# Kernel tuning notes

Hardware: AMD Instinct MI355X
Metric: run time of the kernel (lower is better)

## Reference

```python
import jax, jax.numpy as jnp
import numpy as np

B, T, D, H = 32, 1024, 512, 512


def setup_inputs() -> dict:
    key = jax.random.key(0)
    k = jax.random.split(key, 5)
    s = 1.0 / np.sqrt(H)  # PyTorch LSTM init scale U(-1/sqrt(H), 1/sqrt(H))
    return {
        "x": jax.random.normal(k[0], (B, T, D), dtype=jnp.float32),
        "W_ih": jax.random.uniform(k[1], (4 * H, D), jnp.float32, -s, s),
        "W_hh": jax.random.uniform(k[2], (4 * H, H), jnp.float32, -s, s),
        "b_ih": jax.random.uniform(k[3], (4 * H,), jnp.float32, -s, s),
        "b_hh": jax.random.uniform(k[4], (4 * H,), jnp.float32, -s, s),
    }


def _lstm(x, W_ih, W_hh, b_ih, b_hh):
    # x: [B, T, D] (batch_first). Precompute input projections for all steps.
    xg = jnp.einsum("btd,gd->btg", x, W_ih) + (b_ih + b_hh)  # [B, T, 4H]
    xg = jnp.transpose(xg, (1, 0, 2))  # [T, B, 4H] time-major for scan

    def step(carry, xg_t):
        h, c = carry  # [B, H] each
        gates = xg_t + h @ W_hh.T  # [B, 4H]
        i, f, g, o = jnp.split(gates, 4, axis=-1)  # PyTorch gate order i,f,g,o
        i = jax.nn.sigmoid(i)
        f = jax.nn.sigmoid(f)
        g = jnp.tanh(g)
        o = jax.nn.sigmoid(o)
        c = f * c + i * g
        h = o * jnp.tanh(c)
        return (h, c), h

    h0 = jnp.zeros((x.shape[0], H), x.dtype)
    c0 = jnp.zeros((x.shape[0], H), x.dtype)
    (h_n, c_n), hs = jax.lax.scan(step, (h0, c0), xg)
    out = jnp.transpose(hs, (1, 0, 2))  # [B, T, H] batch_first output
    return out, h_n[None], c_n[None]  # h_n/c_n: [num_layers=1, B, H]


def reference(x, W_ih, W_hh, b_ih, b_hh):
    # Returns (last_hidden_state, h_n, c_n) matching outputs[0], outputs[1]
    return _lstm(x, W_ih, W_hh, b_ih, b_hh)
```

## Files before the change

kernel.cpp:

```cpp
#include <hip/hip_runtime.h>
#include <stdint.h>

typedef __attribute__((ext_vector_type(4))) float f32x4;
typedef __attribute__((ext_vector_type(8))) short bf16x8;
typedef __attribute__((ext_vector_type(4))) unsigned int u32x4;
typedef __attribute__((ext_vector_type(2))) unsigned int u32x2;
typedef __attribute__((ext_vector_type(4))) unsigned short u16x4;
typedef unsigned short ushort_t;

#define B_N 32
#define T_N 1024
#define D_N 512
#define H_N 512
#define G4H 2048

__device__ __forceinline__ ushort_t f2bf(float f) {
    union { float f; unsigned int u; } v; v.f = f;
    unsigned int r = v.u + 0x7FFFu + ((v.u >> 16) & 1u);
    return (ushort_t)(r >> 16);
}
__device__ __forceinline__ float bf2f(ushort_t b) {
    union { unsigned int u; float f; } v; v.u = ((unsigned int)b) << 16;
    return v.f;
}
__device__ __forceinline__ float fsig(float x) {
    return __builtin_amdgcn_rcpf(1.f + __expf(-x));
}
__device__ __forceinline__ float ftanh(float x) {
    return 1.f - 2.f * __builtin_amdgcn_rcpf(1.f + __expf(2.f * x));
}

__global__ __launch_bounds__(256) void prep_kernel(
    const float* __restrict__ wih, const float* __restrict__ whh,
    const float* __restrict__ bih, const float* __restrict__ bhh,
    ushort_t* __restrict__ wihb, ushort_t* __restrict__ whhb,
    float* __restrict__ bias, unsigned int* __restrict__ ringu)
{
    size_t i = (size_t)blockIdx.x * 256 + threadIdx.x;
    if (i < 2048) bias[i] = bih[i] + bhh[i];
    if (i < 32768) ringu[i] = 0u;
    const size_t NW = (size_t)G4H * D_N / 4;
    if (i < NW) {
        f32x4 v = ((const f32x4*)wih)[i];
        u16x4 o; o[0]=f2bf(v[0]); o[1]=f2bf(v[1]); o[2]=f2bf(v[2]); o[3]=f2bf(v[3]);
        ((u16x4*)wihb)[i] = o;
    } else if (i < 2 * NW) {
        size_t j = i - NW;
        f32x4 v = ((const f32x4*)whh)[j];
        u16x4 o; o[0]=f2bf(v[0]); o[1]=f2bf(v[1]); o[2]=f2bf(v[2]); o[3]=f2bf(v[3]);
        ((u16x4*)whhb)[j] = o;
    }
}

__global__ __launch_bounds__(512, 1) void xg_gemm(
    const float* __restrict__ x,
    const ushort_t* __restrict__ wihb,
    const float* __restrict__ bias,
    ushort_t* __restrict__ xg)
{
    const int tc = blockIdx.x >> 3;
    const int gb = blockIdx.x & 7;
    const int tid = threadIdx.x;
    const int w = tid >> 6, l = tid & 63, lr = l & 15, lk = l >> 4;

    __shared__ ushort_t xs[16 * 520];

    const int r0 = gb * 256 + w * 16;
    const int r1 = r0 + 128;
    bf16x8 a0[16], a1[16];
#pragma unroll
    for (int kk = 0; kk < 16; ++kk) {
        a0[kk] = *(const bf16x8*)(wihb + (size_t)(r0 + lr) * D_N + kk * 32 + lk * 8);
        a1[kk] = *(const bf16x8*)(wihb + (size_t)(r1 + lr) * D_N + kk * 32 + lk * 8);
    }
    float bs0[4], bs1[4];
#pragma unroll
    for (int j = 0; j < 4; ++j) {
        bs0[j] = bias[r0 + lk * 4 + j];
        bs1[j] = bias[r1 + lk * 4 + j];
    }

    const int srow = tid >> 5;
    const int sq   = tid & 31;

    for (int b = 0; b < B_N; ++b) {
        const float* xr = x + ((size_t)b * T_N + tc * 16 + srow) * D_N;
#pragma unroll
        for (int c = 0; c < 4; ++c) {
            f32x4 v = *(const f32x4*)(xr + c * 128 + sq * 4);
            u16x4 o; o[0]=f2bf(v[0]); o[1]=f2bf(v[1]); o[2]=f2bf(v[2]); o[3]=f2bf(v[3]);
            *(u16x4*)(xs + srow * 520 + c * 128 + sq * 4) = o;
        }
        __syncthreads();

        f32x4 c0, c1;
#pragma unroll
        for (int j = 0; j < 4; ++j) { c0[j] = 0.f; c1[j] = 0.f; }
#pragma unroll
        for (int kk = 0; kk < 16; ++kk) {
            bf16x8 bf = *(const bf16x8*)((const char*)xs + lr * 1040 + kk * 64 + lk * 16);
            c0 = __builtin_amdgcn_mfma_f32_16x16x32_bf16(a0[kk], bf, c0, 0, 0, 0);
            c1 = __builtin_amdgcn_mfma_f32_16x16x32_bf16(a1[kk], bf, c1, 0, 0, 0);
        }

        const int t = tc * 16 + lr;
        ushort_t* op = xg + (size_t)t * (B_N * G4H) + (size_t)b * G4H;
        u16x4 o0, o1;
#pragma unroll
        for (int j = 0; j < 4; ++j) {
            o0[j] = f2bf(c0[j] + bs0[j]);
            o1[j] = f2bf(c1[j] + bs1[j]);
        }
        *(u16x4*)(op + r0 + lk * 4) = o0;
        *(u16x4*)(op + r1 + lk * 4) = o1;
        __syncthreads();
    }
}

__global__ __launch_bounds__(512, 1) void lstm_rec(
    const ushort_t* __restrict__ xg,
    const ushort_t* __restrict__ whhb,
    unsigned int* __restrict__ ringu,
    float* __restrict__ out,
    float* __restrict__ hn,
    float* __restrict__ cn)
{
    const int tid = threadIdx.x;
    const int g = blockIdx.x >> 4;
    const int s = blockIdx.x & 15;
    const int w = tid >> 6, l = tid & 63, lr = l & 15, lk = l >> 4;

    __shared__ ushort_t hstage[4][544];

    const int col4 = s * 32 + w * 4;
    const int gc = (lr >> 2) * 512 + col4 + (lr & 3);
    bf16x8 wfrag[16];
#pragma unroll
    for (int kk = 0; kk < 16; ++kk)
        wfrag[kk] = *(const bf16x8*)(whhb + (size_t)gc * H_N + kk * 32 + lk * 8);

    float c_reg[4] = {0.f, 0.f, 0.f, 0.f};
    unsigned int* ringg = ringu + g * 4096;
    const ushort_t* xgp = xg + (size_t)(g * 4) * G4H + gc;

    for (int t = 0; t < T_N; ++t) {
        const ushort_t* xa = xgp + (size_t)t * (B_N * G4H);
        f32x4 acc0, acc1;
#pragma unroll
        for (int j = 0; j < 4; ++j) {
            acc0[j] = bf2f(xa[(size_t)j * G4H]);
            acc1[j] = 0.f;
        }

        if (t > 0) {
            if (tid < 64) {
                const unsigned int* pp0 = ringg + ((t - 1) & 1) * 2048 + l * 8;
                const unsigned int* pp1 = pp0 + 1024;
                const unsigned int tp = ((unsigned int)t) << 16;
                u32x4 a[8];
                int guard = 0;
                for (;;) {
                    asm volatile(
                        "global_load_dwordx4 %0, %8, off sc0 sc1\n\t"
                        "global_load_dwordx4 %1, %8, off offset:16 sc0 sc1\n\t"
                        "global_load_dwordx4 %2, %8, off offset:2048 sc0 sc1\n\t"
                        "global_load_dwordx4 %3, %8, off offset:2064 sc0 sc1\n\t"
                        "global_load_dwordx4 %4, %9, off sc0 sc1\n\t"
                        "global_load_dwordx4 %5, %9, off offset:16 sc0 sc1\n\t"
                        "global_load_dwordx4 %6, %9, off offset:2048 sc0 sc1\n\t"
                        "global_load_dwordx4 %7, %9, off offset:2064 sc0 sc1\n\t"
                        "s_waitcnt vmcnt(0)"
                        : "=&v"(a[0]), "=&v"(a[1]), "=&v"(a[2]), "=&v"(a[3]),
                          "=&v"(a[4]), "=&v"(a[5]), "=&v"(a[6]), "=&v"(a[7])
                        : "v"(pp0), "v"(pp1)
                        : "memory");
                    unsigned int d = 0;
#pragma unroll
                    for (int r = 0; r < 8; ++r) {
                        d |= (a[r][0] ^ tp); d |= (a[r][1] ^ tp);
                        d |= (a[r][2] ^ tp); d |= (a[r][3] ^ tp);
                    }
                    int ok = ((d & 0xFFFF0000u) == 0u);
                    if (__all(ok) || ++guard > (1 << 16)) break;
                    __builtin_amdgcn_s_sleep(1);
                }
#pragma unroll
                for (int n = 0; n < 4; ++n) {
                    u32x4 p;
                    p[0] = __builtin_amdgcn_perm(a[2*n][1], a[2*n][0], 0x05040100u);
                    p[1] = __builtin_amdgcn_perm(a[2*n][3], a[2*n][2], 0x05040100u);
                    p[2] = __builtin_amdgcn_perm(a[2*n+1][1], a[2*n+1][0], 0x05040100u);
                    p[3] = __builtin_amdgcn_perm(a[2*n+1][3], a[2*n+1][2], 0x05040100u);
                    *(u32x4*)((char*)hstage + n * 1088 + l * 16) = p;
                }
            }
            __syncthreads();

            const char* ap = (const char*)hstage + (lr & 3) * 1088 + lk * 16;
#pragma unroll
            for (int kk = 0; kk < 16; ++kk) {
                bf16x8 af = *(const bf16x8*)(ap + kk * 64);
                if (kk & 1)
                    acc1 = __builtin_amdgcn_mfma_f32_16x16x32_bf16(af, wfrag[kk], acc1, 0, 0, 0);
                else
                    acc0 = __builtin_amdgcn_mfma_f32_16x16x32_bf16(af, wfrag[kk], acc0, 0, 0, 0);
            }
        } else {
            __syncthreads();
        }

#pragma unroll
        for (int j = 0; j < 4; ++j) acc0[j] += acc1[j];

        const int q = (l >> 2) & 3;
        float av[4];
#pragma unroll
        for (int j = 0; j < 4; ++j)
            av[j] = (q == 2) ? ftanh(acc0[j]) : fsig(acc0[j]);

        float hv[4];
#pragma unroll
        for (int j = 0; j < 4; ++j) {
            float f_ = __shfl_xor(av[j], 4);
            float g_ = __shfl_xor(av[j], 8);
            float o_ = __shfl_xor(av[j], 12);
            c_reg[j] = f_ * c_reg[j] + av[j] * g_;
            hv[j] = o_ * ftanh(c_reg[j]);
        }

        if (l < 4) {
            unsigned int* rp = ringg + (t & 1) * 2048 + col4 + l;
            const unsigned int tag = ((unsigned int)(t + 1)) << 16;
#pragma unroll
            for (int j = 0; j < 4; ++j) {
                unsigned int hw = tag | (unsigned int)f2bf(hv[j]);
                asm volatile("global_store_dword %0, %1, off sc0 sc1"
                             :: "v"(rp + j * 512), "v"(hw) : "memory");
            }
            float* op = out + (size_t)(g * 4) * T_N * H_N + (size_t)t * H_N + col4 + l;
#pragma unroll
            for (int j = 0; j < 4; ++j)
                op[(size_t)j * T_N * H_N] = hv[j];
            if (t == T_N - 1) {
#pragma unroll
                for (int j = 0; j < 4; ++j) {
                    size_t bi = (size_t)(g * 4 + j) * H_N + col4 + l;
                    hn[bi] = hv[j];
                    cn[bi] = c_reg[j];
                }
            }
        }
    }
}

extern "C" void kernel_launch(void* const* d_in, const int* in_sizes, int n_in,
                              void* d_out, int out_size, void* d_ws, size_t ws_size,
                              hipStream_t stream) {
    (void)in_sizes; (void)n_in; (void)out_size; (void)ws_size;
    const float* x   = (const float*)d_in[0];
    const float* wih = (const float*)d_in[1];
    const float* whh = (const float*)d_in[2];
    const float* bih = (const float*)d_in[3];
    const float* bhh = (const float*)d_in[4];
    float* out = (float*)d_out;
    float* hn  = out + (size_t)B_N * T_N * H_N;
    float* cn  = hn + (size_t)B_N * H_N;

    char* ws = (char*)d_ws;
    ushort_t*     xg    = (ushort_t*)    (ws);
    ushort_t*     wihb  = (ushort_t*)    (ws + 167772160);
    ushort_t*     whhb  = (ushort_t*)    (ws + 169869312);
    float*        bias  = (float*)       (ws + 171966464);
    unsigned int* ringu = (unsigned int*)(ws + 171974656);

    prep_kernel<<<2048, 256, 0, stream>>>(wih, whh, bih, bhh,
                                          wihb, whhb, bias, ringu);
    xg_gemm<<<512, 512, 0, stream>>>(x, wihb, bias, xg);
    lstm_rec<<<128, 512, 0, stream>>>(xg, whhb, ringu, out, hn, cn);
}
```

Before: 2.276 ms.

## Prefetch ring loads and next-step input gates before spin-wait

Issues the ring-buffer loads for the next timestep's hidden state right after storing the current h, and checks them at the top of the next step before falling back to the spin loop. Also prefetches the next step's precomputed input-gate values into registers. The MFMA accumulation is split across four independent accumulators instead of two to shorten dependency chains. The intent is to hide global-load and polling latency on the recurrent critical path. The prefetched ring loads may often return stale tags and trigger the retry path anyway, and the extra registers raise pressure.

```diff
diff --git a/kernel.cpp b/kernel.cpp
--- a/kernel.cpp
+++ b/kernel.cpp
@@ -143,46 +143,62 @@
     unsigned int* ringg = ringu + g * 4096;
     const ushort_t* xgp = xg + (size_t)(g * 4) * G4H + gc;
 
+    u32x4 a[8];
+    ushort_t xw[4];
+#pragma unroll
+    for (int j = 0; j < 4; ++j) xw[j] = xgp[(size_t)j * G4H];
+
     for (int t = 0; t < T_N; ++t) {
-        const ushort_t* xa = xgp + (size_t)t * (B_N * G4H);
-        f32x4 acc0, acc1;
+        f32x4 acc0, acc1, acc2, acc3;
 #pragma unroll
         for (int j = 0; j < 4; ++j) {
-            acc0[j] = bf2f(xa[(size_t)j * G4H]);
-            acc1[j] = 0.f;
+            acc0[j] = bf2f(xw[j]);
+            acc1[j] = 0.f; acc2[j] = 0.f; acc3[j] = 0.f;
         }
 
         if (t > 0) {
             if (tid < 64) {
-                const unsigned int* pp0 = ringg + ((t - 1) & 1) * 2048 + l * 8;
-                const unsigned int* pp1 = pp0 + 1024;
+                asm volatile("s_waitcnt vmcnt(0)"
+                             : "+v"(a[0]), "+v"(a[1]), "+v"(a[2]), "+v"(a[3]),
+                               "+v"(a[4]), "+v"(a[5]), "+v"(a[6]), "+v"(a[7])
+                             :: "memory");
                 const unsigned int tp = ((unsigned int)t) << 16;
-                u32x4 a[8];
-                int guard = 0;
-                for (;;) {
-                    asm volatile(
-                        "global_load_dwordx4 %0, %8, off sc0 sc1\n\t"
-                        "global_load_dwordx4 %1, %8, off offset:16 sc0 sc1\n\t"
-                        "global_load_dwordx4 %2, %8, off offset:2048 sc0 sc1\n\t"
-                        "global_load_dwordx4 %3, %8, off offset:2064 sc0 sc1\n\t"
-                        "global_load_dwordx4 %4, %9, off sc0 sc1\n\t"
-                        "global_load_dwordx4 %5, %9, off offset:16 sc0 sc1\n\t"
-                        "global_load_dwordx4 %6, %9, off offset:2048 sc0 sc1\n\t"
-                        "global_load_dwordx4 %7, %9, off offset:2064 sc0 sc1\n\t"
-                        "s_waitcnt vmcnt(0)"
-                        : "=&v"(a[0]), "=&v"(a[1]), "=&v"(a[2]), "=&v"(a[3]),
-                          "=&v"(a[4]), "=&v"(a[5]), "=&v"(a[6]), "=&v"(a[7])
-                        : "v"(pp0), "v"(pp1)
-                        : "memory");
-                    unsigned int d = 0;
-#pragma unroll
-                    for (int r = 0; r < 8; ++r) {
-                        d |= (a[r][0] ^ tp); d |= (a[r][1] ^ tp);
-                        d |= (a[r][2] ^ tp); d |= (a[r][3] ^ tp);
+                unsigned int d = 0;
+#pragma unroll
+                for (int r = 0; r < 8; ++r) {
+                    d |= (a[r][0] ^ tp); d |= (a[r][1] ^ tp);
+                    d |= (a[r][2] ^ tp); d |= (a[r][3] ^ tp);
+                }
+                int ok = ((d & 0xFFFF0000u) == 0u);
+                if (!__all(ok)) {
+                    const unsigned int* pp0 = ringg + ((t - 1) & 1) * 2048 + l * 8;
+                    const unsigned int* pp1 = pp0 + 1024;
+                    int guard = 0;
+                    for (;;) {
+                        __builtin_amdgcn_s_sleep(1);
+                        asm volatile(
+                            "global_load_dwordx4 %0, %8, off sc0 sc1\n\t"
+                            "global_load_dwordx4 %1, %8, off offset:16 sc0 sc1\n\t"
+                            "global_load_dwordx4 %2, %8, off offset:2048 sc0 sc1\n\t"
+                            "global_load_dwordx4 %3, %8, off offset:2064 sc0 sc1\n\t"
+                            "global_load_dwordx4 %4, %9, off sc0 sc1\n\t"
+                            "global_load_dwordx4 %5, %9, off offset:16 sc0 sc1\n\t"
+                            "global_load_dwordx4 %6, %9, off offset:2048 sc0 sc1\n\t"
+                            "global_load_dwordx4 %7, %9, off offset:2064 sc0 sc1\n\t"
+                            "s_waitcnt vmcnt(0)"
+                            : "=&v"(a[0]), "=&v"(a[1]), "=&v"(a[2]), "=&v"(a[3]),
+                              "=&v"(a[4]), "=&v"(a[5]), "=&v"(a[6]), "=&v"(a[7])
+                            : "v"(pp0), "v"(pp1)
+                            : "memory");
+                        d = 0;
+#pragma unroll
+                        for (int r = 0; r < 8; ++r) {
+                            d |= (a[r][0] ^ tp); d |= (a[r][1] ^ tp);
+                            d |= (a[r][2] ^ tp); d |= (a[r][3] ^ tp);
+                        }
+                        ok = ((d & 0xFFFF0000u) == 0u);
+                        if (__all(ok) || ++guard > (1 << 16)) break;
                     }
-                    int ok = ((d & 0xFFFF0000u) == 0u);
-                    if (__all(ok) || ++guard > (1 << 16)) break;
-                    __builtin_amdgcn_s_sleep(1);
                 }
 #pragma unroll
                 for (int n = 0; n < 4; ++n) {
@@ -200,17 +216,20 @@
 #pragma unroll
             for (int kk = 0; kk < 16; ++kk) {
                 bf16x8 af = *(const bf16x8*)(ap + kk * 64);
-                if (kk & 1)
-                    acc1 = __builtin_amdgcn_mfma_f32_16x16x32_bf16(af, wfrag[kk], acc1, 0, 0, 0);
-                else
-                    acc0 = __builtin_amdgcn_mfma_f32_16x16x32_bf16(af, wfrag[kk], acc0, 0, 0, 0);
+                switch (kk & 3) {
+                case 0: acc0 = __builtin_amdgcn_mfma_f32_16x16x32_bf16(af, wfrag[kk], acc0, 0, 0, 0); break;
+                case 1: acc1 = __builtin_amdgcn_mfma_f32_16x16x32_bf16(af, wfrag[kk], acc1, 0, 0, 0); break;
+                case 2: acc2 = __builtin_amdgcn_mfma_f32_16x16x32_bf16(af, wfrag[kk], acc2, 0, 0, 0); break;
+                default: acc3 = __builtin_amdgcn_mfma_f32_16x16x32_bf16(af, wfrag[kk], acc3, 0, 0, 0); break;
+                }
             }
         } else {
             __syncthreads();
         }
 
 #pragma unroll
-        for (int j = 0; j < 4; ++j) acc0[j] += acc1[j];
+        for (int j = 0; j < 4; ++j)
+            acc0[j] += (acc1[j] + acc2[j]) + acc3[j];
 
         const int q = (l >> 2) & 3;
         float av[4];
@@ -249,6 +268,29 @@
                     cn[bi] = c_reg[j];
                 }
             }
+        }
+
+        if (t < T_N - 1) {
+            if (tid < 64) {
+                const unsigned int* q0 = ringg + (t & 1) * 2048 + l * 8;
+                const unsigned int* q1 = q0 + 1024;
+                asm volatile(
+                    "global_load_dwordx4 %0, %8, off sc0 sc1\n\t"
+                    "global_load_dwordx4 %1, %8, off offset:16 sc0 sc1\n\t"
+                    "global_load_dwordx4 %2, %8, off offset:2048 sc0 sc1\n\t"
+                    "global_load_dwordx4 %3, %8, off offset:2064 sc0 sc1\n\t"
+                    "global_load_dwordx4 %4, %9, off sc0 sc1\n\t"
+                    "global_load_dwordx4 %5, %9, off offset:16 sc0 sc1\n\t"
+                    "global_load_dwordx4 %6, %9, off offset:2048 sc0 sc1\n\t"
+                    "global_load_dwordx4 %7, %9, off offset:2064 sc0 sc1"
+                    : "=&v"(a[0]), "=&v"(a[1]), "=&v"(a[2]), "=&v"(a[3]),
+                      "=&v"(a[4]), "=&v"(a[5]), "=&v"(a[6]), "=&v"(a[7])
+                    : "v"(q0), "v"(q1)
+                    : "memory");
+            }
+            const ushort_t* xa = xgp + (size_t)(t + 1) * (B_N * G4H);
+#pragma unroll
+            for (int j = 0; j < 4; ++j) xw[j] = xa[(size_t)j * G4H];
         }
     }
 }
```

Result: slower. 3.562 ms (+56.5%).
